# Optimization experiments

Hardware: AMD Instinct MI355X
Metric: run time of the kernel (lower is better)

The kernel has to match this reference:

```python
import jax, jax.numpy as jnp
import numpy as np

B_, N_, D_ = 32, 128, 512
H, W = 16, 8
DI, DS, DR = 1024, 16, 32  # d_inner, d_state, dt_rank


def setup_inputs() -> dict:
    key = jax.random.key(0)
    ks = jax.random.split(key, 16)
    f = lambda i, sh, s=1.0: jax.random.normal(ks[i], sh, jnp.float32) * s
    return {
        'r': f(0, (B_, N_, D_)),
        'n': f(1, (B_, N_, D_)),
        't': f(2, (B_, N_, D_)),
        'in_proj_w': f(3, (3, 2 * DI, D_), 0.02),
        'conv_w': f(4, (3, DI, 1, 3, 3), 0.2),
        'conv_b': f(5, (3, DI), 0.02),
        'bn_gamma': jax.random.uniform(ks[6], (3, DI), jnp.float32),
        'bn_beta': f(7, (3, DI), 0.02),
        'bn_mean': jnp.zeros((3, DI), jnp.float32),
        'bn_var': jnp.ones((3, DI), jnp.float32),
        'ssm_xproj_w': f(8, (6, DR + 2 * DS, DI), 0.02),
        'ssm_dt_w': f(9, (6, DI, DR), 0.1),
        'ssm_dt_b': f(10, (6, DI), 1.0),
        'ssm_A_log': jax.random.uniform(ks[11], (6, DI, DS), jnp.float32),
        'ssm_D': jnp.ones((6, DI), jnp.float32),
        'ssm_ln_g': jnp.ones((6, DI), jnp.float32),
        'ssm_ln_b': jnp.zeros((6, DI), jnp.float32),
        'out_proj_w': f(12, (D_, DI), 0.02),
    }


def dwconv_bn_silu(x, w, cb, gm, bt, mn, vr):
    # x: (B, DI, H, W); depthwise 3x3 conv + eval-mode BN + SiLU
    y = jax.lax.conv_general_dilated(x, w, (1, 1), 'SAME', feature_group_count=DI)
    y = y + cb[None, :, None, None]
    y = (y - mn[None, :, None, None]) * (gm / jnp.sqrt(vr + 1e-5))[None, :, None, None] + bt[None, :, None, None]
    return y * jax.nn.sigmoid(y)


def ssm_branch(x, xw, dtw, dtb, A_log, Dp, g, b):
    # selective scan; x: (B, L, DI)
    xd = x @ xw.T                                   # (B,L,DR+2*DS)
    dt, Bm, Cm = xd[..., :DR], xd[..., DR:DR + DS], xd[..., DR + DS:]
    delta = jax.nn.softplus(dt @ dtw.T + dtb)       # (B,L,DI)
    A = -jnp.exp(A_log)                             # (DI,DS)

    def step(h, ins):
        d_t, B_t, C_t, u_t = ins                    # (B,DI),(B,DS),(B,DS),(B,DI)
        dA = jnp.exp(d_t[:, :, None] * A)           # (B,DI,DS)
        h = dA * h + (d_t * u_t)[:, :, None] * B_t[:, None, :]
        y = jnp.einsum('bdn,bn->bd', h, C_t)
        return h, y

    h0 = jnp.zeros((x.shape[0], DI, DS), x.dtype)
    xs = (delta.transpose(1, 0, 2), Bm.transpose(1, 0, 2), Cm.transpose(1, 0, 2), x.transpose(1, 0, 2))
    _, ys = jax.lax.scan(step, h0, xs)              # ys: (L,B,DI)
    y = ys.transpose(1, 0, 2) + x * Dp
    mu = y.mean(-1, keepdims=True)
    var = ((y - mu) ** 2).mean(-1, keepdims=True)
    return (y - mu) / jnp.sqrt(var + 1e-5) * g + b


def reference(r, n, t, in_proj_w, conv_w, conv_b, bn_gamma, bn_beta, bn_mean, bn_var,
              ssm_xproj_w, ssm_dt_w, ssm_dt_b, ssm_A_log, ssm_D, ssm_ln_g, ssm_ln_b, out_proj_w):
    Bb, Nn, Dd = r.shape
    ins = jnp.stack([r, n, t])                      # (3,B,N,D)
    xz = jnp.einsum('mbnd,med->mbne', ins, in_proj_w)
    x, z = xz[..., :DI], xz[..., DI:]
    xs_conv = []
    for m in range(3):                              # 3 modalities, structurally distinct convs
        xm = x[m].reshape(Bb, H, W, DI).transpose(0, 3, 1, 2)
        ym = dwconv_bn_silu(xm, conv_w[m], conv_b[m], bn_gamma[m], bn_beta[m], bn_mean[m], bn_var[m])
        xs_conv.append(ym.transpose(0, 2, 3, 1).reshape(Bb, Nn, DI))
    x_r, x_n, x_t = xs_conv
    # 6 branches: forward r/n/t then time-flipped r/n/t
    xs6 = jnp.stack([x_r, x_n, x_t, x_r[:, ::-1], x_n[:, ::-1], x_t[:, ::-1]])
    ys = jax.vmap(ssm_branch)(xs6, ssm_xproj_w, ssm_dt_w, ssm_dt_b, ssm_A_log, ssm_D, ssm_ln_g, ssm_ln_b)
    y_r = ys[0] + ys[3][:, ::-1]
    y_n = ys[1] + ys[4][:, ::-1]
    y_t = ys[2] + ys[5][:, ::-1]
    y = jnp.concatenate([y_r, y_n, y_t], axis=1)    # (B,3N,DI)
    zc = jnp.concatenate([z[0], z[1], z[2]], axis=1)
    y = y * (zc * jax.nn.sigmoid(zc))
    out = y @ out_proj_w.T                          # (B,3N,D)
    return (r + out[:, :Nn], n + out[:, Nn:2 * Nn], t + out[:, 2 * Nn:])
```

## Files before the change

### kernel.cpp

```cpp
#include <hip/hip_runtime.h>
#include <hip/hip_bf16.h>
#include <hip/hip_fp16.h>
#include <math.h>

#define NB 32
#define NN 128
#define ND 512
#define NDI 1024
#define NDS 16
#define NDR 32

#define L2E 1.442695040888963f
#define LN2 0.6931471805599453f

#define EXP2(x) __builtin_amdgcn_exp2f(x)
#define LOG2(x) __builtin_amdgcn_logf(x)

typedef __attribute__((ext_vector_type(8))) __bf16 bf16x8;
typedef __attribute__((ext_vector_type(4))) float f32x4;

typedef __attribute__((address_space(3))) void lds_void;
typedef const __attribute__((address_space(1))) void glob_void;

__device__ __forceinline__ void gload16(const void* g, void* l) {
    __builtin_amdgcn_global_load_lds((glob_void*)g, (lds_void*)l, 16, 0, 0);
}

__device__ __forceinline__ unsigned short f2bf(float x) {
    __hip_bfloat16 h = __float2bfloat16(x);
    return *(unsigned short*)&h;
}
__device__ __forceinline__ float bf2f(unsigned short v) {
    return __uint_as_float(((unsigned int)v) << 16);
}
__device__ __forceinline__ float hf2f(unsigned short v) {
    __half h = *(__half*)&v;
    return __half2float(h);
}
__device__ __forceinline__ float sigm(float x) {
    return 1.f / (1.f + EXP2(-x * L2E));
}

__device__ __forceinline__ float pair_sum(float y) {
    const int sw = __builtin_amdgcn_mov_dpp(__float_as_int(y), 0xB1, 0xF, 0xF, true);
    return y + __int_as_float(sw);
}

__global__ __launch_bounds__(256) void k_cvt(
    const float* __restrict__ s, unsigned short* __restrict__ d, int n4)
{
    for (int i = blockIdx.x * 256 + threadIdx.x; i < n4; i += gridDim.x * 256) {
        const float4 v = ((const float4*)s)[i];
        ushort4 o;
        o.x = f2bf(v.x); o.y = f2bf(v.y); o.z = f2bf(v.z); o.w = f2bf(v.w);
        ((ushort4*)d)[i] = o;
    }
}

__global__ __launch_bounds__(256) void k_cvt3(
    const float* __restrict__ rr, const float* __restrict__ nn,
    const float* __restrict__ tt, unsigned short* __restrict__ d, int n4)
{
    const int z = blockIdx.z;
    const float* __restrict__ s = (z == 0) ? rr : (z == 1) ? nn : tt;
    unsigned short* __restrict__ dz = d + (size_t)z * n4 * 4;
    for (int i = blockIdx.x * 256 + threadIdx.x; i < n4; i += gridDim.x * 256) {
        const float4 v = ((const float4*)s)[i];
        ushort4 o;
        o.x = f2bf(v.x); o.y = f2bf(v.y); o.z = f2bf(v.z); o.w = f2bf(v.w);
        ((ushort4*)dz)[i] = o;
    }
}

__global__ __launch_bounds__(256) void k_gemm_inproj(
    const unsigned short* __restrict__ Abf,
    const unsigned short* __restrict__ Wbf,
    float* __restrict__ xb, __hip_bfloat16* __restrict__ zbf)
{
    const int m = blockIdx.z;
    const int row0 = blockIdx.x * 128;
    const int col0 = blockIdx.y * 128;
    const unsigned short* __restrict__ A = Abf + (size_t)m * 4096 * 512;
    const unsigned short* __restrict__ Bw = Wbf + (size_t)m * 2048 * 512;
    const int K = 512;
    const int NT = K / 32;

    const int tid = threadIdx.x;
    const int lane = tid & 63;
    const int wave = tid >> 6;
    const int wr = wave >> 1, wc = wave & 1;
    const int lr16 = lane & 15;
    const int kk8 = (lane >> 4) << 3;

    __shared__ __align__(16) short sA[2][128 * 32];
    __shared__ __align__(16) short sB[2][128 * 32];

    f32x4 acc[4][4];
    #pragma unroll
    for (int i = 0; i < 4; ++i)
        #pragma unroll
        for (int j = 0; j < 4; ++j)
            acc[i][j] = (f32x4){0.f, 0.f, 0.f, 0.f};

    #define STAGE(buf, t)                                                        \
        {                                                                        \
            const int k0 = (t) * 32;                                             \
            _Pragma("unroll")                                                    \
            for (int i = 0; i < 2; ++i) {                                        \
                const int c = i * 256 + tid;                                     \
                const int rowc = c >> 2;                                         \
                const int kc = (c & 3) << 3;                                     \
                gload16(A + (size_t)(row0 + rowc) * K + k0 + kc,                 \
                        &sA[buf][rowc * 32 + kc]);                               \
                gload16(Bw + (size_t)(col0 + rowc) * K + k0 + kc,                \
                        &sB[buf][rowc * 32 + kc]);                               \
            }                                                                    \
        }

    #define COMPUTE(buf)                                                         \
        {                                                                        \
            bf16x8 af[4], bfr[4];                                                \
            _Pragma("unroll")                                                    \
            for (int i = 0; i < 4; ++i) {                                        \
                af[i]  = *(const bf16x8*)&sA[buf][(wr * 64 + i * 16 + lr16) * 32 + kk8]; \
                bfr[i] = *(const bf16x8*)&sB[buf][(wc * 64 + i * 16 + lr16) * 32 + kk8]; \
            }                                                                    \
            _Pragma("unroll")                                                    \
            for (int i = 0; i < 4; ++i)                                          \
                _Pragma("unroll")                                                \
                for (int j = 0; j < 4; ++j)                                      \
                    acc[i][j] = __builtin_amdgcn_mfma_f32_16x16x32_bf16(         \
                        af[i], bfr[j], acc[i][j], 0, 0, 0);                      \
        }

    STAGE(0, 0);
    __syncthreads();
    int cur = 0;
    for (int t = 0; t < NT - 1; ++t) {
        STAGE(cur ^ 1, t + 1);
        COMPUTE(cur);
        __syncthreads();
        cur ^= 1;
    }
    COMPUTE(cur);

    const bool isX = (col0 < 1024);
    #pragma unroll
    for (int i = 0; i < 4; ++i) {
        const int rb = row0 + wr * 64 + i * 16 + ((lane >> 4) << 2);
        #pragma unroll
        for (int j = 0; j < 4; ++j) {
            const int cc = col0 + wc * 64 + j * 16 + lr16;
            #pragma unroll
            for (int r = 0; r < 4; ++r) {
                const float v = acc[i][j][r];
                const int row = rb + r;
                if (isX)
                    xb[((size_t)m * 4096 + row) * 1024 + cc] = v;
                else
                    zbf[((size_t)m * 4096 + row) * 1024 + (cc - 1024)] =
                        __float2bfloat16(v);
            }
        }
    }
    #undef STAGE
    #undef COMPUTE
}

__global__ __launch_bounds__(256) void k_conv(
    const float* __restrict__ x, const float* __restrict__ cw,
    const float* __restrict__ cb, const float* __restrict__ gm,
    const float* __restrict__ bt, const float* __restrict__ mn,
    const float* __restrict__ vr, unsigned short* __restrict__ out)
{
    const int nIdx = blockIdx.x;
    const int b = blockIdx.y;
    const int m = blockIdx.z;
    const int h = nIdx >> 3, w = nIdx & 7;
    const float* __restrict__ xm = x + ((size_t)(m * NB + b)) * NN * NDI;

    #pragma unroll
    for (int q = 0; q < 4; ++q) {
        const int di = (q << 8) + threadIdx.x;
        const float* __restrict__ wp = cw + ((size_t)(m * NDI + di)) * 9;
        float s = 0.f;
        #pragma unroll
        for (int kh = 0; kh < 3; ++kh) {
            const int hh = h + kh - 1;
            if ((unsigned)hh < 16u) {
                #pragma unroll
                for (int kw = 0; kw < 3; ++kw) {
                    const int ww = w + kw - 1;
                    if ((unsigned)ww < 8u)
                        s = fmaf(xm[(size_t)(hh * 8 + ww) * NDI + di],
                                 wp[kh * 3 + kw], s);
                }
            }
        }
        const int c = m * NDI + di;
        const float scale = gm[c] * rsqrtf(vr[c] + 1e-5f);
        const float y = (s + cb[c] - mn[c]) * scale + bt[c];
        out[((size_t)(m * NB + b) * NN + nIdx) * NDI + di] = f2bf(y * sigm(y));
    }
}

__global__ __launch_bounds__(256) void k_xproj(
    const unsigned short* __restrict__ xcbf,
    const unsigned short* __restrict__ xwbf,
    float* __restrict__ xd)
{
    const int s = blockIdx.z;
    const int m = (s >= 3) ? (s - 3) : s;
    const bool rev = s >= 3;
    const unsigned short* __restrict__ A = xcbf + (size_t)m * 4096 * 1024;
    const unsigned short* __restrict__ Bw = xwbf + (size_t)s * 64 * 1024;
    const int row0 = blockIdx.x * 128;
    const int NT = 32;

    const int tid = threadIdx.x;
    const int lane = tid & 63;
    const int wave = tid >> 6;
    const int wr = wave >> 1, wc = wave & 1;
    const int lr16 = lane & 15;
    const int kk8 = (lane >> 4) << 3;

    __shared__ __align__(16) short sA[2][128 * 32];
    __shared__ __align__(16) short sB[2][64 * 32];

    f32x4 acc[4][2];
    #pragma unroll
    for (int i = 0; i < 4; ++i)
        #pragma unroll
        for (int j = 0; j < 2; ++j)
            acc[i][j] = (f32x4){0.f, 0.f, 0.f, 0.f};

    #define STAGEX(buf, t)                                                       \
        {                                                                        \
            const int k0 = (t) * 32;                                             \
            _Pragma("unroll")                                                    \
            for (int i = 0; i < 2; ++i) {                                        \
                const int c = i * 256 + tid;                                     \
                const int rowc = c >> 2;                                         \
                const int kc = (c & 3) << 3;                                     \
                const int arow = row0 + rowc;                                    \
                const int ab = arow >> 7, at = arow & 127;                       \
                const int srow = ab * NN + (rev ? (NN - 1 - at) : at);           \
                gload16(A + (size_t)srow * 1024 + k0 + kc,                       \
                        &sA[buf][rowc * 32 + kc]);                               \
            }                                                                    \
            {                                                                    \
                const int rowc = tid >> 2;                                       \
                const int kc = (tid & 3) << 3;                                   \
                gload16(Bw + (size_t)rowc * 1024 + k0 + kc,                      \
                        &sB[buf][rowc * 32 + kc]);                               \
            }                                                                    \
        }

    #define COMPUTEX(buf)                                                        \
        {                                                                        \
            bf16x8 af[4], bfr[2];                                                \
            _Pragma("unroll")                                                    \
            for (int i = 0; i < 4; ++i)                                          \
                af[i] = *(const bf16x8*)&sA[buf][(wr * 64 + i * 16 + lr16) * 32 + kk8]; \
            _Pragma("unroll")                                                    \
            for (int j = 0; j < 2; ++j)                                          \
                bfr[j] = *(const bf16x8*)&sB[buf][(wc * 32 + j * 16 + lr16) * 32 + kk8]; \
            _Pragma("unroll")                                                    \
            for (int i = 0; i < 4; ++i)                                          \
                _Pragma("unroll")                                                \
                for (int j = 0; j < 2; ++j)                                      \
                    acc[i][j] = __builtin_amdgcn_mfma_f32_16x16x32_bf16(         \
                        af[i], bfr[j], acc[i][j], 0, 0, 0);                      \
        }

    STAGEX(0, 0);
    __syncthreads();
    int cur = 0;
    for (int t = 0; t < NT - 1; ++t) {
        STAGEX(cur ^ 1, t + 1);
        COMPUTEX(cur);
        __syncthreads();
        cur ^= 1;
    }
    COMPUTEX(cur);

    #pragma unroll
    for (int i = 0; i < 4; ++i) {
        const int rb = row0 + wr * 64 + i * 16 + ((lane >> 4) << 2);
        #pragma unroll
        for (int j = 0; j < 2; ++j) {
            const int cc = wc * 32 + j * 16 + lr16;
            #pragma unroll
            for (int r = 0; r < 4; ++r) {
                const int row = rb + r;
                xd[((size_t)s * 4096 + row) * 64 + cc] = acc[i][j][r];
            }
        }
    }
    #undef STAGEX
    #undef COMPUTEX
}

__global__ __launch_bounds__(256) void k_delta(
    const float* __restrict__ xd, const float* __restrict__ dtw,
    const float* __restrict__ dtb, unsigned short* __restrict__ deltaT)
{
    const int s = blockIdx.z, b = blockIdx.y;
    const int d = blockIdx.x * 256 + threadIdx.x;

    float wdt[NDR];
    const float* __restrict__ wp = dtw + ((size_t)s * NDI + d) * NDR;
    #pragma unroll
    for (int r = 0; r < NDR; r += 4)
        *(float4*)&wdt[r] = *(const float4*)(wp + r);
    const float bias = dtb[s * NDI + d];

    const float* __restrict__ xrow = xd + ((size_t)(s * NB + b)) * NN * 64;
    unsigned short* __restrict__ dout =
        deltaT + (((size_t)(s * NB + b)) * NDI + d) * NN;

    for (int t8 = 0; t8 < NN / 8; ++t8) {
        ushort4 o0, o1;
        unsigned short* op0 = (unsigned short*)&o0;
        unsigned short* op1 = (unsigned short*)&o1;
        #pragma unroll
        for (int k = 0; k < 8; ++k) {
            const int t = t8 * 8 + k;
            const float* __restrict__ xr = xrow + (size_t)t * 64;
            float dl = bias;
            #pragma unroll
            for (int q = 0; q < 8; ++q) {
                const float4 v = *(const float4*)(xr + q * 4);
                dl = fmaf(v.x, wdt[q * 4 + 0], dl);
                dl = fmaf(v.y, wdt[q * 4 + 1], dl);
                dl = fmaf(v.z, wdt[q * 4 + 2], dl);
                dl = fmaf(v.w, wdt[q * 4 + 3], dl);
            }
            const float e = EXP2(-fabsf(dl) * L2E);
            const float dlt = fmaxf(dl, 0.f) + LOG2(1.f + e) * LN2;
            const __half hv = __float2half(dlt);
            if (k < 4) op0[k] = *(const unsigned short*)&hv;
            else       op1[k - 4] = *(const unsigned short*)&hv;
        }
        *(ushort4*)(dout + t8 * 8) = o0;
        *(ushort4*)(dout + t8 * 8 + 4) = o1;
    }
}

__global__ __launch_bounds__(256) void k_scan(
    const unsigned short* __restrict__ xcbf, const float* __restrict__ xd,
    const unsigned short* __restrict__ deltaT,
    const float* __restrict__ alog, const float* __restrict__ Dp,
    float* __restrict__ y6)
{
    const int s = blockIdx.z, b = blockIdx.y;
    const int tid = threadIdx.x;
    const int jg = tid & 1;
    const int d = blockIdx.x * 128 + (tid >> 1);
    const int m = (s >= 3) ? (s - 3) : s;
    const bool rev = s >= 3;

    float a2[8], h[8];
    const float* __restrict__ ap = alog + ((size_t)s * NDI + d) * NDS + jg * 8;
    #pragma unroll
    for (int j = 0; j < 8; j += 4) {
        const float4 v = *(const float4*)(ap + j);
        a2[j]     = -EXP2(v.x * L2E) * L2E;
        a2[j + 1] = -EXP2(v.y * L2E) * L2E;
        a2[j + 2] = -EXP2(v.z * L2E) * L2E;
        a2[j + 3] = -EXP2(v.w * L2E) * L2E;
        h[j] = h[j + 1] = h[j + 2] = h[j + 3] = 0.f;
    }
    const float Dd = Dp[s * NDI + d];

    const unsigned short* __restrict__ up =
        xcbf + ((size_t)(m * NB + b)) * NN * NDI + d;
    const float* __restrict__ xr =
        xd + ((size_t)(s * NB + b)) * NN * 64 + 32 + jg * 8;
    const unsigned short* __restrict__ dpT =
        deltaT + (((size_t)(s * NB + b)) * NDI + d) * NN;
    float* __restrict__ yp = y6 + ((size_t)(s * NB + b)) * NN * NDI + d;

    int un = (rev ? (NN - 1) : 0) * NDI;
    const int ustep = rev ? -NDI : NDI;
    const bool writer = (jg == 0);

    uint4 dv  = *(const uint4*)dpT;
    uint4 dvn = *(const uint4*)(dpT + 8);
    float u = bf2f(up[un]); un += ustep;
    float4 B0 = *(const float4*)(xr);
    float4 B1 = *(const float4*)(xr + 4);
    float4 C0 = *(const float4*)(xr + 16);
    float4 C1 = *(const float4*)(xr + 20);

    for (int t8 = 0; t8 < NN / 8; ++t8) {
        #pragma unroll
        for (int k = 0; k < 8; ++k) {
            const float* __restrict__ xn = xr + 64;
            const float4 nB0 = *(const float4*)(xn);
            const float4 nB1 = *(const float4*)(xn + 4);
            const float4 nC0 = *(const float4*)(xn + 16);
            const float4 nC1 = *(const float4*)(xn + 20);
            const float u_n = bf2f(up[un]); un += ustep;

            const float delta = hf2f(((const unsigned short*)&dv)[k]);
            const float du = delta * u;
            float y = 0.f;
            #pragma unroll
            for (int j = 0; j < 4; ++j) {
                const float dA = EXP2(delta * a2[j]);
                h[j] = fmaf(dA, h[j], du * ((const float*)&B0)[j]);
                y = fmaf(h[j], ((const float*)&C0)[j], y);
            }
            #pragma unroll
            for (int j = 0; j < 4; ++j) {
                const float dA = EXP2(delta * a2[4 + j]);
                h[4 + j] = fmaf(dA, h[4 + j], du * ((const float*)&B1)[j]);
                y = fmaf(h[4 + j], ((const float*)&C1)[j], y);
            }
            y = pair_sum(y);
            if (writer) yp[(size_t)(t8 * 8 + k) * NDI] = fmaf(u, Dd, y);

            u = u_n; B0 = nB0; B1 = nB1; C0 = nC0; C1 = nC1; xr = xn;
        }
        dv = dvn;
        dvn = *(const uint4*)(dpT + (t8 + 2) * 8);
    }
}

__global__ __launch_bounds__(256) void k_combine(
    const float* __restrict__ y6, const __hip_bfloat16* __restrict__ zbf,
    const float* __restrict__ g, const float* __restrict__ be,
    __hip_bfloat16* __restrict__ yg)
{
    const int t = blockIdx.x, b = blockIdx.y, m = blockIdx.z;
    const int tid = threadIdx.x;
    const int dd = tid << 2;
    const float* __restrict__ rowf = y6 + ((size_t)(m * NB + b) * NN + t) * NDI;
    const float* __restrict__ rowr =
        y6 + ((size_t)((m + 3) * NB + b) * NN + (NN - 1 - t)) * NDI;
    const __hip_bfloat16* __restrict__ zrow =
        zbf + ((size_t)(m * NB + b) * NN + t) * NDI;

    const float4 vf = *(const float4*)(rowf + dd);
    const float4 vr = *(const float4*)(rowr + dd);
    float sf = vf.x + vf.y + vf.z + vf.w;
    float qf = vf.x * vf.x + vf.y * vf.y + vf.z * vf.z + vf.w * vf.w;
    float sr = vr.x + vr.y + vr.z + vr.w;
    float qr = vr.x * vr.x + vr.y * vr.y + vr.z * vr.z + vr.w * vr.w;

    #pragma unroll
    for (int off = 32; off > 0; off >>= 1) {
        sf += __shfl_down(sf, off, 64);
        qf += __shfl_down(qf, off, 64);
        sr += __shfl_down(sr, off, 64);
        qr += __shfl_down(qr, off, 64);
    }
    __shared__ float red[4][4];
    const int wv = tid >> 6;
    if ((tid & 63) == 0) { red[wv][0] = sf; red[wv][1] = qf; red[wv][2] = sr; red[wv][3] = qr; }
    __syncthreads();
    const float tsf = red[0][0] + red[1][0] + red[2][0] + red[3][0];
    const float tqf = red[0][1] + red[1][1] + red[2][1] + red[3][1];
    const float tsr = red[0][2] + red[1][2] + red[2][2] + red[3][2];
    const float tqr = red[0][3] + red[1][3] + red[2][3] + red[3][3];
    const float muf = tsf * (1.f / NDI);
    const float varf = tqf * (1.f / NDI) - muf * muf;
    const float rsf = rsqrtf(varf + 1e-5f);
    const float mur = tsr * (1.f / NDI);
    const float varr = tqr * (1.f / NDI) - mur * mur;
    const float rsr = rsqrtf(varr + 1e-5f);

    const float4 gf = *(const float4*)(g + m * NDI + dd);
    const float4 bf = *(const float4*)(be + m * NDI + dd);
    const float4 gr = *(const float4*)(g + (m + 3) * NDI + dd);
    const float4 br = *(const float4*)(be + (m + 3) * NDI + dd);
    const ushort4 zu = *(const ushort4*)(zrow + dd);

    float lf[4], lr2[4], zv[4];
    lf[0] = (vf.x - muf) * rsf * gf.x + bf.x;
    lf[1] = (vf.y - muf) * rsf * gf.y + bf.y;
    lf[2] = (vf.z - muf) * rsf * gf.z + bf.z;
    lf[3] = (vf.w - muf) * rsf * gf.w + bf.w;
    lr2[0] = (vr.x - mur) * rsr * gr.x + br.x;
    lr2[1] = (vr.y - mur) * rsr * gr.y + br.y;
    lr2[2] = (vr.z - mur) * rsr * gr.z + br.z;
    lr2[3] = (vr.w - mur) * rsr * gr.w + br.w;
    zv[0] = bf2f(zu.x);
    zv[1] = bf2f(zu.y);
    zv[2] = bf2f(zu.z);
    zv[3] = bf2f(zu.w);

    ushort4 o;
    unsigned short* op = (unsigned short*)&o;
    #pragma unroll
    for (int q = 0; q < 4; ++q) {
        op[q] = f2bf((lf[q] + lr2[q]) * zv[q] * sigm(zv[q]));
    }
    *(ushort4*)(yg + ((size_t)(m * NB + b) * NN + t) * NDI + dd) = o;
}

__global__ __launch_bounds__(256) void k_gemm_outproj(
    const unsigned short* __restrict__ Abf,
    const unsigned short* __restrict__ Wbf,
    const float* __restrict__ rr, const float* __restrict__ nn,
    const float* __restrict__ tt, float* __restrict__ out)
{
    const int row0 = blockIdx.x * 128;
    const int col0 = blockIdx.y * 128;
    const int K = 1024;
    const int NT = K / 32;

    const int tid = threadIdx.x;
    const int lane = tid & 63;
    const int wave = tid >> 6;
    const int wr = wave >> 1, wc = wave & 1;
    const int lr16 = lane & 15;
    const int kk8 = (lane >> 4) << 3;

    __shared__ __align__(16) short sA[2][128 * 32];
    __shared__ __align__(16) short sB[2][128 * 32];

    f32x4 acc[4][4];
    #pragma unroll
    for (int i = 0; i < 4; ++i)
        #pragma unroll
        for (int j = 0; j < 4; ++j)
            acc[i][j] = (f32x4){0.f, 0.f, 0.f, 0.f};

    #define STAGE(buf, t)                                                        \
        {                                                                        \
            const int k0 = (t) * 32;                                             \
            _Pragma("unroll")                                                    \
            for (int i = 0; i < 2; ++i) {                                        \
                const int c = i * 256 + tid;                                     \
                const int rowc = c >> 2;                                         \
                const int kc = (c & 3) << 3;                                     \
                gload16(Abf + (size_t)(row0 + rowc) * K + k0 + kc,               \
                        &sA[buf][rowc * 32 + kc]);                               \
                gload16(Wbf + (size_t)(col0 + rowc) * K + k0 + kc,               \
                        &sB[buf][rowc * 32 + kc]);                               \
            }                                                                    \
        }

    #define COMPUTE(buf)                                                         \
        {                                                                        \
            bf16x8 af[4], bfr[4];                                                \
            _Pragma("unroll")                                                    \
            for (int i = 0; i < 4; ++i) {                                        \
                af[i]  = *(const bf16x8*)&sA[buf][(wr * 64 + i * 16 + lr16) * 32 + kk8]; \
                bfr[i] = *(const bf16x8*)&sB[buf][(wc * 64 + i * 16 + lr16) * 32 + kk8]; \
            }                                                                    \
            _Pragma("unroll")                                                    \
            for (int i = 0; i < 4; ++i)                                          \
                _Pragma("unroll")                                                \
                for (int j = 0; j < 4; ++j)                                      \
                    acc[i][j] = __builtin_amdgcn_mfma_f32_16x16x32_bf16(         \
                        af[i], bfr[j], acc[i][j], 0, 0, 0);                      \
        }

    STAGE(0, 0);
    __syncthreads();
    int cur = 0;
    for (int t = 0; t < NT - 1; ++t) {
        STAGE(cur ^ 1, t + 1);
        COMPUTE(cur);
        __syncthreads();
        cur ^= 1;
    }
    COMPUTE(cur);

    const int m = row0 >> 12;
    const float* __restrict__ resid = (m == 0) ? rr : (m == 1) ? nn : tt;
    #pragma unroll
    for (int i = 0; i < 4; ++i) {
        const int rb = row0 + wr * 64 + i * 16 + ((lane >> 4) << 2);
        #pragma unroll
        for (int j = 0; j < 4; ++j) {
            const int cc = col0 + wc * 64 + j * 16 + lr16;
            #pragma unroll
            for (int r = 0; r < 4; ++r) {
                const int row = rb + r;
                const int bt = row & 4095;
                out[(size_t)row * ND + cc] =
                    acc[i][j][r] + resid[(size_t)bt * ND + cc];
            }
        }
    }
    #undef STAGE
    #undef COMPUTE
}

extern "C" void kernel_launch(void* const* d_in, const int* in_sizes, int n_in,
                              void* d_out, int out_size, void* d_ws, size_t ws_size,
                              hipStream_t stream) {
    const float* rr   = (const float*)d_in[0];
    const float* nn   = (const float*)d_in[1];
    const float* tt   = (const float*)d_in[2];
    const float* wip  = (const float*)d_in[3];
    const float* cw   = (const float*)d_in[4];
    const float* cb   = (const float*)d_in[5];
    const float* gm   = (const float*)d_in[6];
    const float* bt   = (const float*)d_in[7];
    const float* mn   = (const float*)d_in[8];
    const float* vr   = (const float*)d_in[9];
    const float* xw   = (const float*)d_in[10];
    const float* dtw  = (const float*)d_in[11];
    const float* dtb  = (const float*)d_in[12];
    const float* alog = (const float*)d_in[13];
    const float* Dp   = (const float*)d_in[14];
    const float* lng  = (const float*)d_in[15];
    const float* lnb  = (const float*)d_in[16];
    const float* wout = (const float*)d_in[17];
    float* out = (float*)d_out;

    uint8_t* p = (uint8_t*)d_ws;
    unsigned short* Abf    = (unsigned short*)p;  p += (size_t)3 * 4096 * 512 * 2;
    unsigned short* Wbf    = (unsigned short*)p;  p += (size_t)3 * 2048 * 512 * 2;
    unsigned short* Woutbf = (unsigned short*)p;  p += (size_t)512 * 1024 * 2;
    unsigned short* Xwbf   = (unsigned short*)p;  p += (size_t)6 * 64 * 1024 * 2;
    float*          xb     = (float*)p;           p += (size_t)3 * 4096 * 1024 * 4;
    __hip_bfloat16* zbf    = (__hip_bfloat16*)p;  p += (size_t)3 * 4096 * 1024 * 2;
    unsigned short* xcbf   = (unsigned short*)p;  p += (size_t)3 * 4096 * 1024 * 2;
    float*          xdb    = (float*)p;           p += (size_t)6 * 4096 * 64 * 4;
    float*          y6     = (float*)p;           p += (size_t)6 * 4096 * 1024 * 4;
    unsigned short* deltaT = (unsigned short*)xb;
    __hip_bfloat16* ygbf   = (__hip_bfloat16*)xb;

    k_cvt3<<<dim3(2048, 1, 3), 256, 0, stream>>>(rr, nn, tt, Abf, 4096 * 512 / 4);
    k_cvt<<<dim3(2048), 256, 0, stream>>>(wip,  Wbf, 3 * 2048 * 512 / 4);
    k_cvt<<<dim3(512),  256, 0, stream>>>(wout, Woutbf, 512 * 1024 / 4);
    k_cvt<<<dim3(384),  256, 0, stream>>>(xw,   Xwbf, 6 * 64 * 1024 / 4);

    k_gemm_inproj<<<dim3(32, 16, 3), 256, 0, stream>>>(Abf, Wbf, xb, zbf);
    k_conv<<<dim3(128, 32, 3), 256, 0, stream>>>(xb, cw, cb, gm, bt, mn, vr, xcbf);
    k_xproj<<<dim3(32, 1, 6), 256, 0, stream>>>(xcbf, Xwbf, xdb);
    k_delta<<<dim3(4, 32, 6), 256, 0, stream>>>(xdb, dtw, dtb, deltaT);
    k_scan<<<dim3(8, 32, 6), 256, 0, stream>>>(xcbf, xdb, deltaT, alog, Dp, y6);
    k_combine<<<dim3(128, 32, 3), 256, 0, stream>>>(y6, zbf, lng, lnb, ygbf);
    k_gemm_outproj<<<dim3(96, 4, 1), 256, 0, stream>>>(
        (const unsigned short*)ygbf, Woutbf, rr, nn, tt, out);
}
```

Measured before the change: 541.3 us.

## Fuse depthwise conv into in-proj GEMM epilogue and store scan output as bf16

The in-projection GEMM now stages its x tile (one full batch image of 128 tokens by 128 channels) into LDS as fp16 with a swizzle. It then applies the 3x3 depthwise conv, BN and SiLU directly in the epilogue, removing the fp32 x round trip and the separate conv kernel. The scan output y6 is also written as bf16 instead of fp32, halving its write and read traffic in k_combine. The trade-offs are reduced precision (fp16 intermediate x, bf16 scan output) and extra LDS traffic and sync in the GEMM epilogue.

```diff
diff --git a/kernel.cpp b/kernel.cpp
--- a/kernel.cpp
+++ b/kernel.cpp
@@ -36,6 +36,10 @@
 __device__ __forceinline__ float hf2f(unsigned short v) {
     __half h = *(__half*)&v;
     return __half2float(h);
+}
+__device__ __forceinline__ unsigned short f2hf(float x) {
+    __half h = __float2half(x);
+    return *(unsigned short*)&h;
 }
 __device__ __forceinline__ float sigm(float x) {
     return 1.f / (1.f + EXP2(-x * L2E));
@@ -72,10 +76,13 @@
     }
 }
 
-__global__ __launch_bounds__(256) void k_gemm_inproj(
+__global__ __launch_bounds__(256) void k_gemm_inproj_conv(
     const unsigned short* __restrict__ Abf,
     const unsigned short* __restrict__ Wbf,
-    float* __restrict__ xb, __hip_bfloat16* __restrict__ zbf)
+    const float* __restrict__ cw, const float* __restrict__ cbb,
+    const float* __restrict__ gm, const float* __restrict__ bt,
+    const float* __restrict__ mn, const float* __restrict__ vr,
+    unsigned short* __restrict__ xcbf, __hip_bfloat16* __restrict__ zbf)
 {
     const int m = blockIdx.z;
     const int row0 = blockIdx.x * 128;
@@ -92,8 +99,9 @@
     const int lr16 = lane & 15;
     const int kk8 = (lane >> 4) << 3;
 
-    __shared__ __align__(16) short sA[2][128 * 32];
-    __shared__ __align__(16) short sB[2][128 * 32];
+    __shared__ __align__(16) short smem[16384];
+    short (*sA)[128 * 32] = (short(*)[128 * 32])smem;
+    short (*sB)[128 * 32] = (short(*)[128 * 32])(smem + 8192);
 
     f32x4 acc[4][4];
     #pragma unroll
@@ -144,64 +152,81 @@
     }
     COMPUTE(cur);
 
-    const bool isX = (col0 < 1024);
-    #pragma unroll
-    for (int i = 0; i < 4; ++i) {
-        const int rb = row0 + wr * 64 + i * 16 + ((lane >> 4) << 2);
+    if (col0 < 1024) {
+        __syncthreads();
+        ushort* ct = (ushort*)smem;
+        #pragma unroll
+        for (int i = 0; i < 4; ++i) {
+            #pragma unroll
+            for (int j = 0; j < 4; ++j) {
+                #pragma unroll
+                for (int r = 0; r < 4; ++r) {
+                    const int t = wr * 64 + i * 16 + ((lane >> 4) << 2) + r;
+                    const int c = wc * 64 + j * 16 + lr16;
+                    ct[t * 128 + (c ^ ((t & 31) << 1))] = f2hf(acc[i][j][r]);
+                }
+            }
+        }
+        __syncthreads();
+        const int b = blockIdx.x;
+        unsigned short* __restrict__ orow =
+            xcbf + ((size_t)(m * NB + b)) * NN * NDI + col0;
         #pragma unroll
         for (int j = 0; j < 4; ++j) {
-            const int cc = col0 + wc * 64 + j * 16 + lr16;
-            #pragma unroll
-            for (int r = 0; r < 4; ++r) {
-                const float v = acc[i][j][r];
-                const int row = rb + r;
-                if (isX)
-                    xb[((size_t)m * 4096 + row) * 1024 + cc] = v;
-                else
+            const int c = wc * 64 + j * 16 + lr16;
+            const int cidx = m * NDI + col0 + c;
+            const float* __restrict__ wp = cw + (size_t)cidx * 9;
+            float w9[9];
+            #pragma unroll
+            for (int k = 0; k < 9; ++k) w9[k] = wp[k];
+            const float scale = gm[cidx] * rsqrtf(vr[cidx] + 1e-5f);
+            const float shift = (cbb[cidx] - mn[cidx]) * scale + bt[cidx];
+            #pragma unroll
+            for (int i = 0; i < 4; ++i) {
+                #pragma unroll
+                for (int r = 0; r < 4; ++r) {
+                    const int t = wr * 64 + i * 16 + ((lane >> 4) << 2) + r;
+                    const int h = t >> 3, w = t & 7;
+                    float s = 0.f;
+                    #pragma unroll
+                    for (int kh = 0; kh < 3; ++kh) {
+                        const int hh = h + kh - 1;
+                        if ((unsigned)hh < 16u) {
+                            #pragma unroll
+                            for (int kw = 0; kw < 3; ++kw) {
+                                const int ww = w + kw - 1;
+                                if ((unsigned)ww < 8u) {
+                                    const int tt = hh * 8 + ww;
+                                    const unsigned short uv =
+                                        ct[tt * 128 + (c ^ ((tt & 31) << 1))];
+                                    s = fmaf(hf2f(uv), w9[kh * 3 + kw], s);
+                                }
+                            }
+                        }
+                    }
+                    const float y = fmaf(s, scale, shift);
+                    orow[(size_t)t * NDI + c] = f2bf(y * sigm(y));
+                }
+            }
+        }
+    } else {
+        #pragma unroll
+        for (int i = 0; i < 4; ++i) {
+            const int rb = row0 + wr * 64 + i * 16 + ((lane >> 4) << 2);
+            #pragma unroll
+            for (int j = 0; j < 4; ++j) {
+                const int cc = col0 + wc * 64 + j * 16 + lr16;
+                #pragma unroll
+                for (int r = 0; r < 4; ++r) {
+                    const int row = rb + r;
                     zbf[((size_t)m * 4096 + row) * 1024 + (cc - 1024)] =
-                        __float2bfloat16(v);
+                        __float2bfloat16(acc[i][j][r]);
+                }
             }
         }
     }
     #undef STAGE
     #undef COMPUTE
-}
-
-__global__ __launch_bounds__(256) void k_conv(
-    const float* __restrict__ x, const float* __restrict__ cw,
-    const float* __restrict__ cb, const float* __restrict__ gm,
-    const float* __restrict__ bt, const float* __restrict__ mn,
-    const float* __restrict__ vr, unsigned short* __restrict__ out)
-{
-    const int nIdx = blockIdx.x;
-    const int b = blockIdx.y;
-    const int m = blockIdx.z;
-    const int h = nIdx >> 3, w = nIdx & 7;
-    const float* __restrict__ xm = x + ((size_t)(m * NB + b)) * NN * NDI;
-
-    #pragma unroll
-    for (int q = 0; q < 4; ++q) {
-        const int di = (q << 8) + threadIdx.x;
-        const float* __restrict__ wp = cw + ((size_t)(m * NDI + di)) * 9;
-        float s = 0.f;
-        #pragma unroll
-        for (int kh = 0; kh < 3; ++kh) {
-            const int hh = h + kh - 1;
-            if ((unsigned)hh < 16u) {
-                #pragma unroll
-                for (int kw = 0; kw < 3; ++kw) {
-                    const int ww = w + kw - 1;
-                    if ((unsigned)ww < 8u)
-                        s = fmaf(xm[(size_t)(hh * 8 + ww) * NDI + di],
-                                 wp[kh * 3 + kw], s);
-                }
-            }
-        }
-        const int c = m * NDI + di;
-        const float scale = gm[c] * rsqrtf(vr[c] + 1e-5f);
-        const float y = (s + cb[c] - mn[c]) * scale + bt[c];
-        out[((size_t)(m * NB + b) * NN + nIdx) * NDI + di] = f2bf(y * sigm(y));
-    }
 }
 
 __global__ __launch_bounds__(256) void k_xproj(
@@ -338,9 +363,8 @@
             }
             const float e = EXP2(-fabsf(dl) * L2E);
             const float dlt = fmaxf(dl, 0.f) + LOG2(1.f + e) * LN2;
-            const __half hv = __float2half(dlt);
-            if (k < 4) op0[k] = *(const unsigned short*)&hv;
-            else       op1[k - 4] = *(const unsigned short*)&hv;
+            if (k < 4) op0[k] = f2hf(dlt);
+            else       op1[k - 4] = f2hf(dlt);
         }
         *(ushort4*)(dout + t8 * 8) = o0;
         *(ushort4*)(dout + t8 * 8 + 4) = o1;
@@ -351,7 +375,7 @@
     const unsigned short* __restrict__ xcbf, const float* __restrict__ xd,
     const unsigned short* __restrict__ deltaT,
     const float* __restrict__ alog, const float* __restrict__ Dp,
-    float* __restrict__ y6)
+    unsigned short* __restrict__ y6)
 {
     const int s = blockIdx.z, b = blockIdx.y;
     const int tid = threadIdx.x;
@@ -379,7 +403,8 @@
         xd + ((size_t)(s * NB + b)) * NN * 64 + 32 + jg * 8;
     const unsigned short* __restrict__ dpT =
         deltaT + (((size_t)(s * NB + b)) * NDI + d) * NN;
-    float* __restrict__ yp = y6 + ((size_t)(s * NB + b)) * NN * NDI + d;
+    unsigned short* __restrict__ yp =
+        y6 + ((size_t)(s * NB + b)) * NN * NDI + d;
 
     int un = (rev ? (NN - 1) : 0) * NDI;
     const int ustep = rev ? -NDI : NDI;
@@ -419,7 +444,7 @@
                 y = fmaf(h[4 + j], ((const float*)&C1)[j], y);
             }
             y = pair_sum(y);
-            if (writer) yp[(size_t)(t8 * 8 + k) * NDI] = fmaf(u, Dd, y);
+            if (writer) yp[(size_t)(t8 * 8 + k) * NDI] = f2bf(fmaf(u, Dd, y));
 
             u = u_n; B0 = nB0; B1 = nB1; C0 = nC0; C1 = nC1; xr = xn;
         }
@@ -429,25 +454,32 @@
 }
 
 __global__ __launch_bounds__(256) void k_combine(
-    const float* __restrict__ y6, const __hip_bfloat16* __restrict__ zbf,
+    const unsigned short* __restrict__ y6, const __hip_bfloat16* __restrict__ zbf,
     const float* __restrict__ g, const float* __restrict__ be,
     __hip_bfloat16* __restrict__ yg)
 {
     const int t = blockIdx.x, b = blockIdx.y, m = blockIdx.z;
     const int tid = threadIdx.x;
     const int dd = tid << 2;
-    const float* __restrict__ rowf = y6 + ((size_t)(m * NB + b) * NN + t) * NDI;
-    const float* __restrict__ rowr =
+    const unsigned short* __restrict__ rowf =
+        y6 + ((size_t)(m * NB + b) * NN + t) * NDI;
+    const unsigned short* __restrict__ rowr =
         y6 + ((size_t)((m + 3) * NB + b) * NN + (NN - 1 - t)) * NDI;
     const __hip_bfloat16* __restrict__ zrow =
         zbf + ((size_t)(m * NB + b) * NN + t) * NDI;
 
-    const float4 vf = *(const float4*)(rowf + dd);
-    const float4 vr = *(const float4*)(rowr + dd);
-    float sf = vf.x + vf.y + vf.z + vf.w;
-    float qf = vf.x * vf.x + vf.y * vf.y + vf.z * vf.z + vf.w * vf.w;
-    float sr = vr.x + vr.y + vr.z + vr.w;
-    float qr = vr.x * vr.x + vr.y * vr.y + vr.z * vr.z + vr.w * vr.w;
+    const ushort4 vfu = *(const ushort4*)(rowf + dd);
+    const ushort4 vru = *(const ushort4*)(rowr + dd);
+    float vf[4], vr2[4];
+    vf[0] = bf2f(vfu.x); vf[1] = bf2f(vfu.y); vf[2] = bf2f(vfu.z); vf[3] = bf2f(vfu.w);
+    vr2[0] = bf2f(vru.x); vr2[1] = bf2f(vru.y); vr2[2] = bf2f(vru.z); vr2[3] = bf2f(vru.w);
+
+    float sf = 0.f, qf = 0.f, sr = 0.f, qr = 0.f;
+    #pragma unroll
+    for (int q = 0; q < 4; ++q) {
+        sf += vf[q]; qf = fmaf(vf[q], vf[q], qf);
+        sr += vr2[q]; qr = fmaf(vr2[q], vr2[q], qr);
+    }
 
     #pragma unroll
     for (int off = 32; off > 0; off >>= 1) {
@@ -478,14 +510,14 @@
     const ushort4 zu = *(const ushort4*)(zrow + dd);
 
     float lf[4], lr2[4], zv[4];
-    lf[0] = (vf.x - muf) * rsf * gf.x + bf.x;
-    lf[1] = (vf.y - muf) * rsf * gf.y + bf.y;
-    lf[2] = (vf.z - muf) * rsf * gf.z + bf.z;
-    lf[3] = (vf.w - muf) * rsf * gf.w + bf.w;
-    lr2[0] = (vr.x - mur) * rsr * gr.x + br.x;
-    lr2[1] = (vr.y - mur) * rsr * gr.y + br.y;
-    lr2[2] = (vr.z - mur) * rsr * gr.z + br.z;
-    lr2[3] = (vr.w - mur) * rsr * gr.w + br.w;
+    lf[0] = (vf[0] - muf) * rsf * gf.x + bf.x;
+    lf[1] = (vf[1] - muf) * rsf * gf.y + bf.y;
+    lf[2] = (vf[2] - muf) * rsf * gf.z + bf.z;
+    lf[3] = (vf[3] - muf) * rsf * gf.w + bf.w;
+    lr2[0] = (vr2[0] - mur) * rsr * gr.x + br.x;
+    lr2[1] = (vr2[1] - mur) * rsr * gr.y + br.y;
+    lr2[2] = (vr2[2] - mur) * rsr * gr.z + br.z;
+    lr2[3] = (vr2[3] - mur) * rsr * gr.w + br.w;
     zv[0] = bf2f(zu.x);
     zv[1] = bf2f(zu.y);
     zv[2] = bf2f(zu.z);
@@ -619,25 +651,24 @@
     unsigned short* Wbf    = (unsigned short*)p;  p += (size_t)3 * 2048 * 512 * 2;
     unsigned short* Woutbf = (unsigned short*)p;  p += (size_t)512 * 1024 * 2;
     unsigned short* Xwbf   = (unsigned short*)p;  p += (size_t)6 * 64 * 1024 * 2;
-    float*          xb     = (float*)p;           p += (size_t)3 * 4096 * 1024 * 4;
     __hip_bfloat16* zbf    = (__hip_bfloat16*)p;  p += (size_t)3 * 4096 * 1024 * 2;
     unsigned short* xcbf   = (unsigned short*)p;  p += (size_t)3 * 4096 * 1024 * 2;
     float*          xdb    = (float*)p;           p += (size_t)6 * 4096 * 64 * 4;
-    float*          y6     = (float*)p;           p += (size_t)6 * 4096 * 1024 * 4;
-    unsigned short* deltaT = (unsigned short*)xb;
-    __hip_bfloat16* ygbf   = (__hip_bfloat16*)xb;
+    unsigned short* y6bf   = (unsigned short*)p;  p += (size_t)6 * 4096 * 1024 * 2;
+    unsigned short* deltaT = (unsigned short*)p;  p += (size_t)6 * 4096 * 1024 * 2;
+    __hip_bfloat16* ygbf   = (__hip_bfloat16*)p;  p += (size_t)3 * 4096 * 1024 * 2;
 
     k_cvt3<<<dim3(2048, 1, 3), 256, 0, stream>>>(rr, nn, tt, Abf, 4096 * 512 / 4);
     k_cvt<<<dim3(2048), 256, 0, stream>>>(wip,  Wbf, 3 * 2048 * 512 / 4);
     k_cvt<<<dim3(512),  256, 0, stream>>>(wout, Woutbf, 512 * 1024 / 4);
     k_cvt<<<dim3(384),  256, 0, stream>>>(xw,   Xwbf, 6 * 64 * 1024 / 4);
 
-    k_gemm_inproj<<<dim3(32, 16, 3), 256, 0, stream>>>(Abf, Wbf, xb, zbf);
-    k_conv<<<dim3(128, 32, 3), 256, 0, stream>>>(xb, cw, cb, gm, bt, mn, vr, xcbf);
+    k_gemm_inproj_conv<<<dim3(32, 16, 3), 256, 0, stream>>>(
+        Abf, Wbf, cw, cb, gm, bt, mn, vr, xcbf, zbf);
     k_xproj<<<dim3(32, 1, 6), 256, 0, stream>>>(xcbf, Xwbf, xdb);
     k_delta<<<dim3(4, 32, 6), 256, 0, stream>>>(xdb, dtw, dtb, deltaT);
-    k_scan<<<dim3(8, 32, 6), 256, 0, stream>>>(xcbf, xdb, deltaT, alog, Dp, y6);
-    k_combine<<<dim3(128, 32, 3), 256, 0, stream>>>(y6, zbf, lng, lnb, ygbf);
+    k_scan<<<dim3(8, 32, 6), 256, 0, stream>>>(xcbf, xdb, deltaT, alog, Dp, y6bf);
+    k_combine<<<dim3(128, 32, 3), 256, 0, stream>>>(y6bf, zbf, lng, lnb, ygbf);
     k_gemm_outproj<<<dim3(96, 4, 1), 256, 0, stream>>>(
         (const unsigned short*)ygbf, Woutbf, rr, nn, tt, out);
 }
```

Measured after the change: 437.0 us. 1.24x faster.
